# Performance work log

Hardware: AMD Instinct MI355X
Metric: run time of the kernel (lower is better)

## Reference

```python
import jax, jax.numpy as jnp
import numpy as np

N, D, E, L, H, F1, G, A = 4096, 256, 131072, 3, 4, 128, 16, 32

def setup_inputs() -> dict:
    key = jax.random.key(0)
    ks = jax.random.split(key, 12)
    s = lambda k, shape, fan: jax.random.normal(k, shape, jnp.float32) / np.sqrt(fan)
    return {
        "x": jax.random.normal(ks[0], (N, D), jnp.float32),
        "edge_attr": jax.random.uniform(ks[1], (E,), jnp.float32),
        "conv_Wself": s(ks[2], (L, D, D), D),
        "conv_Wnbr": s(ks[3], (L, D, D), D),
        "conv_b": jnp.zeros((L, D), jnp.float32),
        "bn_gamma": jnp.ones((L - 1, D), jnp.float32),
        "bn_beta": jnp.zeros((L - 1, D), jnp.float32),
        "bn_mean": jnp.zeros((L - 1, D), jnp.float32),
        "bn_var": jnp.ones((L - 1, D), jnp.float32),
        "Wqkv": s(ks[4], (3, D, D), D),
        "bqkv": jnp.zeros((3, D), jnp.float32),
        "Wo": s(ks[5], (D, D), D),
        "bo": jnp.zeros((D,), jnp.float32),
        "fc1_W": s(ks[6], (D, F1), D),
        "fc1_b": jnp.zeros((F1,), jnp.float32),
        "AW1": s(ks[7], (G, F1, A), F1),
        "Ab1": jnp.zeros((G, A), jnp.float32),
        "AW2": s(ks[8], (G, A, 1), A),
        "Ab2": jnp.zeros((G, 1), jnp.float32),
        "edge_index": jax.random.randint(ks[9], (2, E), 0, N, jnp.int32),
        "node_groups": jax.random.randint(ks[10], (N,), 0, G, jnp.int32),
    }


def reference(x, edge_attr, conv_Wself, conv_Wnbr, conv_b, bn_gamma, bn_beta,
              bn_mean, bn_var, Wqkv, bqkv, Wo, bo, fc1_W, fc1_b,
              AW1, Ab1, AW2, Ab2, edge_index, node_groups):
    src, dst = edge_index[0], edge_index[1]
    # message-passing conv stack (edge_attr only used by the last, non-attention layer)
    for i in range(L):
        msg = x[src]
        if i == L - 1:
            msg = msg * edge_attr[:, None]
        agg = jax.ops.segment_sum(msg, dst, num_segments=N)
        x = x @ conv_Wself[i] + agg @ conv_Wnbr[i] + conv_b[i]
        if i < L - 1:
            x = bn_gamma[i] * (x - bn_mean[i]) * jax.lax.rsqrt(bn_var[i] + 1e-5) + bn_beta[i]
            x = jax.nn.elu(x)
    # hierarchy self-attention over all N nodes (batch of 1), residual add
    dh = D // H
    q = (x @ Wqkv[0] + bqkv[0]).reshape(N, H, dh)
    k = (x @ Wqkv[1] + bqkv[1]).reshape(N, H, dh)
    v = (x @ Wqkv[2] + bqkv[2]).reshape(N, H, dh)
    scores = jnp.einsum('nhd,mhd->hnm', q, k) / np.sqrt(dh).astype(np.float32)
    attn = jax.nn.softmax(scores, axis=-1)
    o = jnp.einsum('hnm,mhd->nhd', attn, v).reshape(N, D) @ Wo + bo
    x = x + o
    feats = jax.nn.elu(x @ fc1_W + fc1_b)  # [N, F1]; dropout is eval no-op
    # MoE-style per-node group adapter routing: gather tiny MLP weights per node
    h = jax.nn.relu(jnp.einsum('nd,nda->na', feats, AW1[node_groups]) + Ab1[node_groups])
    out = jnp.einsum('na,nao->no', h, AW2[node_groups]) + Ab2[node_groups]  # [N, 1]
    return out
```

## Files before the change

kernel.cpp:

```cpp
#include <hip/hip_runtime.h>
#include <math.h>

#define NN   4096
#define DIM  256
#define NE   131072
#define NH   4
#define DH   64
#define F1D  128
#define NG   16
#define AD   32

typedef unsigned short u16;
typedef unsigned int   u32;
typedef _Float16 f16;
typedef __attribute__((ext_vector_type(8))) _Float16 half8;
typedef __attribute__((ext_vector_type(4))) float f32x4;

enum { EPI_BIAS = 0, EPI_BNELU = 1 };
enum { MEPI_WO = 0, MEPI_FC1 = 1 };

#define MFMA16(a, b, c) __builtin_amdgcn_mfma_f32_16x16x32_f16(a, b, c, 0, 0, 0)

__device__ inline u16 f2h(float x) { union { f16 f; u16 u; } c; c.f = (f16)x; return c.u; }
__device__ inline void split16(float x, u16& h, u16& l) {
    union { f16 f; u16 u; } ch, cl;
    ch.f = (f16)x;
    cl.f = (f16)(x - (float)ch.f);
    h = ch.u; l = cl.u;
}

__global__ void csr_count(const int* __restrict__ dst, int* __restrict__ cnt) {
    int e = blockIdx.x * 256 + threadIdx.x;
    atomicAdd(&cnt[dst[e]], 1);
}

__global__ __launch_bounds__(1024) void csr_scan(
    int* __restrict__ cnt, int* __restrict__ off)
{
    __shared__ int wsum[16];
    const int t = threadIdx.x;
    const int lane = t & 63;
    int4 v = *(const int4*)&cnt[t * 4];
    const int s = v.x + v.y + v.z + v.w;
    int acc = s;
    #pragma unroll
    for (int o = 1; o < 64; o <<= 1) {
        int u = __shfl_up(acc, o);
        if (lane >= o) acc += u;
    }
    if (lane == 63) wsum[t >> 6] = acc;
    __syncthreads();
    if (t < 16) {
        int w0 = wsum[t];
        int a2 = w0;
        #pragma unroll
        for (int o = 1; o < 16; o <<= 1) {
            int u = __shfl_up(a2, o);
            if (t >= o) a2 += u;
        }
        wsum[t] = a2 - w0;
    }
    __syncthreads();
    const int base = wsum[t >> 6] + (acc - s);
    off[t * 4 + 0] = base;
    off[t * 4 + 1] = base + v.x;
    off[t * 4 + 2] = base + v.x + v.y;
    off[t * 4 + 3] = base + v.x + v.y + v.z;
    *(int4*)&cnt[t * 4] = make_int4(0, 0, 0, 0);
    if (t == 1023) off[NN] = base + s;
}

__global__ void csr_fill(const int* __restrict__ dst, const int* __restrict__ src,
                         const float* __restrict__ eattr, const int* __restrict__ off,
                         int* __restrict__ cur, int* __restrict__ esrc,
                         float* __restrict__ ewt) {
    int e = blockIdx.x * 256 + threadIdx.x;
    int d = dst[e];
    int pos = off[d] + atomicAdd(&cur[d], 1);
    esrc[pos] = src[e];
    ewt[pos]  = eattr[e];
}

__global__ __launch_bounds__(256) void prep_kernel(
    const float* __restrict__ x,
    const float* __restrict__ Ws, const float* __restrict__ Wn,
    const float* __restrict__ Wqkv, const float* __restrict__ Wo,
    const float* __restrict__ fc1W,
    u16* __restrict__ xh, u16* __restrict__ xl,
    u16* __restrict__ wch, u16* __restrict__ wcl,
    u16* __restrict__ w4h, u16* __restrict__ w4l,
    u16* __restrict__ f1h, u16* __restrict__ f1l,
    int* __restrict__ cur)
{
    const int b = blockIdx.x;
    const int t = threadIdx.x;
    if (b < 1024) {
        const int gid = b * 256 + t;
        const float4 v = *(const float4*)&x[(size_t)gid * 4];
        u16 h[4], l[4];
        split16(v.x, h[0], l[0]); split16(v.y, h[1], l[1]);
        split16(v.z, h[2], l[2]); split16(v.w, h[3], l[3]);
        *(uint2*)&xh[(size_t)gid * 4] =
            make_uint2((u32)h[0] | ((u32)h[1] << 16), (u32)h[2] | ((u32)h[3] << 16));
        *(uint2*)&xl[(size_t)gid * 4] =
            make_uint2((u32)l[0] | ((u32)l[1] << 16), (u32)l[2] | ((u32)l[3] << 16));
    } else if (b < 1408) {
        const int gid = (b - 1024) * 256 + t;
        const int L = gid / 32768;
        const int rem = gid % 32768;
        const int m = rem / 128;
        const int k4 = (rem % 128) * 4;
        const float* S = Ws + (size_t)L * 65536;
        const float* Nb = Wn + (size_t)L * 65536;
        u16 h[4], l[4];
        #pragma unroll
        for (int j = 0; j < 4; ++j) {
            const int k = k4 + j;
            const float v = (k < 256) ? S[(size_t)k * 256 + m]
                                      : Nb[(size_t)(k - 256) * 256 + m];
            split16(v, h[j], l[j]);
        }
        const size_t o = (size_t)L * 131072 + (size_t)m * 512 + k4;
        *(uint2*)&wch[o] = make_uint2((u32)h[0] | ((u32)h[1] << 16), (u32)h[2] | ((u32)h[3] << 16));
        *(uint2*)&wcl[o] = make_uint2((u32)l[0] | ((u32)l[1] << 16), (u32)l[2] | ((u32)l[3] << 16));
    } else if (b < 1664) {
        const int gid = (b - 1408) * 256 + t;
        const int mat = gid / 16384;
        const int rem = gid % 16384;
        const int m = rem / 64;
        const int k4 = (rem % 64) * 4;
        const float* W = (mat < 3) ? Wqkv + (size_t)mat * 65536 : Wo;
        u16 h[4], l[4];
        #pragma unroll
        for (int j = 0; j < 4; ++j)
            split16(W[(size_t)(k4 + j) * 256 + m], h[j], l[j]);
        const size_t o = (size_t)mat * 65536 + (size_t)m * 256 + k4;
        *(uint2*)&w4h[o] = make_uint2((u32)h[0] | ((u32)h[1] << 16), (u32)h[2] | ((u32)h[3] << 16));
        *(uint2*)&w4l[o] = make_uint2((u32)l[0] | ((u32)l[1] << 16), (u32)l[2] | ((u32)l[3] << 16));
    } else if (b < 1696) {
        const int gid = (b - 1664) * 256 + t;
        const int m = gid / 64;
        const int k4 = (gid % 64) * 4;
        u16 h[4], l[4];
        #pragma unroll
        for (int j = 0; j < 4; ++j)
            split16(fc1W[(size_t)(k4 + j) * F1D + m], h[j], l[j]);
        const size_t o = (size_t)m * 256 + k4;
        *(uint2*)&f1h[o] = make_uint2((u32)h[0] | ((u32)h[1] << 16), (u32)h[2] | ((u32)h[3] << 16));
        *(uint2*)&f1l[o] = make_uint2((u32)l[0] | ((u32)l[1] << 16), (u32)l[2] | ((u32)l[3] << 16));
    } else {
        const int gid = (b - 1696) * 256 + t;
        if (gid < NN / 4) *(int4*)&cur[gid * 4] = make_int4(0, 0, 0, 0);
    }
}

template<bool LAST>
__global__ __launch_bounds__(256) void agg_kernel(
    const float* __restrict__ x, const int* __restrict__ esrc,
    const float* __restrict__ ewt, const int* __restrict__ off,
    u16* __restrict__ aggh, u16* __restrict__ aggl)
{
    const int node = blockIdx.x * 4 + (threadIdx.x >> 6);
    const int lane = threadIdx.x & 63;
    const int d4 = lane * 4;
    int j = off[node];
    const int j1 = off[node + 1];
    float4 acc = make_float4(0.f, 0.f, 0.f, 0.f);
    for (; j + 4 <= j1; j += 4) {
        const int s0 = esrc[j], s1 = esrc[j + 1], s2 = esrc[j + 2], s3 = esrc[j + 3];
        const float4 x0 = *(const float4*)&x[(size_t)s0 * DIM + d4];
        const float4 x1 = *(const float4*)&x[(size_t)s1 * DIM + d4];
        const float4 x2 = *(const float4*)&x[(size_t)s2 * DIM + d4];
        const float4 x3 = *(const float4*)&x[(size_t)s3 * DIM + d4];
        const float w0 = LAST ? ewt[j]     : 1.f;
        const float w1 = LAST ? ewt[j + 1] : 1.f;
        const float w2 = LAST ? ewt[j + 2] : 1.f;
        const float w3 = LAST ? ewt[j + 3] : 1.f;
        acc.x = fmaf(x0.x, w0, acc.x); acc.y = fmaf(x0.y, w0, acc.y);
        acc.z = fmaf(x0.z, w0, acc.z); acc.w = fmaf(x0.w, w0, acc.w);
        acc.x = fmaf(x1.x, w1, acc.x); acc.y = fmaf(x1.y, w1, acc.y);
        acc.z = fmaf(x1.z, w1, acc.z); acc.w = fmaf(x1.w, w1, acc.w);
        acc.x = fmaf(x2.x, w2, acc.x); acc.y = fmaf(x2.y, w2, acc.y);
        acc.z = fmaf(x2.z, w2, acc.z); acc.w = fmaf(x2.w, w2, acc.w);
        acc.x = fmaf(x3.x, w3, acc.x); acc.y = fmaf(x3.y, w3, acc.y);
        acc.z = fmaf(x3.z, w3, acc.z); acc.w = fmaf(x3.w, w3, acc.w);
    }
    for (; j < j1; ++j) {
        const int s = esrc[j];
        const float w = LAST ? ewt[j] : 1.f;
        const float4 xv = *(const float4*)&x[(size_t)s * DIM + d4];
        acc.x = fmaf(xv.x, w, acc.x); acc.y = fmaf(xv.y, w, acc.y);
        acc.z = fmaf(xv.z, w, acc.z); acc.w = fmaf(xv.w, w, acc.w);
    }
    u16 h[4], l[4];
    split16(acc.x, h[0], l[0]); split16(acc.y, h[1], l[1]);
    split16(acc.z, h[2], l[2]); split16(acc.w, h[3], l[3]);
    *(uint2*)&aggh[(size_t)node * DIM + d4] =
        make_uint2((u32)h[0] | ((u32)h[1] << 16), (u32)h[2] | ((u32)h[3] << 16));
    *(uint2*)&aggl[(size_t)node * DIM + d4] =
        make_uint2((u32)l[0] | ((u32)l[1] << 16), (u32)l[2] | ((u32)l[3] << 16));
}

template<int EPI>
__global__ __launch_bounds__(256) void conv_mfma(
    const u16* __restrict__ xh, const u16* __restrict__ xl,
    const u16* __restrict__ gh, const u16* __restrict__ gl,
    const u16* __restrict__ bth, const u16* __restrict__ btl,
    const float* __restrict__ bias,
    const float* __restrict__ gamma, const float* __restrict__ beta,
    const float* __restrict__ bnmean, const float* __restrict__ bnvar,
    float* __restrict__ outf, u16* __restrict__ oh, u16* __restrict__ ol)
{
    __shared__ u16 lds[13824];
    u16* As_h = lds;
    u16* As_l = lds + 2304;
    u16* Bs_h = lds + 4608;
    u16* Bs_l = lds + 9216;
    #define TKP 72

    const int tid  = threadIdx.x;
    const int row0 = blockIdx.y * 32;
    const int col0 = blockIdx.x * 64;

    const int w   = tid >> 6;
    const int l15 = tid & 15, h4 = (tid & 63) >> 4;
    const int rh  = w & 1, ch = w >> 1;
    const int arow = tid >> 3, acs = (tid & 7) * 8;
    const int brow = tid & 63, bseg = tid >> 6;
    const int bc = bseg * 16;

    uint4 sah, sal, sbh0, sbh1, sbl0, sbl1;
    {
        sah = *((const uint4*)&xh[(size_t)(row0 + arow) * DIM + acs]);
        sal = *((const uint4*)&xl[(size_t)(row0 + arow) * DIM + acs]);
        const u16* pbh = bth + (size_t)(col0 + brow) * 512 + bc;
        const u16* pbl = btl + (size_t)(col0 + brow) * 512 + bc;
        sbh0 = ((const uint4*)pbh)[0]; sbh1 = ((const uint4*)pbh)[1];
        sbl0 = ((const uint4*)pbl)[0]; sbl1 = ((const uint4*)pbl)[1];
    }

    const f32x4 z4 = {0.f, 0.f, 0.f, 0.f};
    f32x4 acc[2] = {z4, z4};

    for (int kt = 0; kt < 8; ++kt) {
        *(uint4*)&As_h[arow * TKP + acs] = sah;
        *(uint4*)&As_l[arow * TKP + acs] = sal;
        *(uint4*)&Bs_h[brow * TKP + bc]     = sbh0;
        *(uint4*)&Bs_h[brow * TKP + bc + 8] = sbh1;
        *(uint4*)&Bs_l[brow * TKP + bc]     = sbl0;
        *(uint4*)&Bs_l[brow * TKP + bc + 8] = sbl1;
        if (kt + 1 < 8) {
            const int kn = kt + 1;
            const u16 *pah, *pal;
            if (kn < 4) {
                pah = xh + (size_t)(row0 + arow) * DIM + kn * 64 + acs;
                pal = xl + (size_t)(row0 + arow) * DIM + kn * 64 + acs;
            } else {
                pah = gh + (size_t)(row0 + arow) * DIM + (kn - 4) * 64 + acs;
                pal = gl + (size_t)(row0 + arow) * DIM + (kn - 4) * 64 + acs;
            }
            sah = *((const uint4*)pah);
            sal = *((const uint4*)pal);
            const u16* pbh = bth + (size_t)(col0 + brow) * 512 + kn * 64 + bc;
            const u16* pbl = btl + (size_t)(col0 + brow) * 512 + kn * 64 + bc;
            sbh0 = ((const uint4*)pbh)[0]; sbh1 = ((const uint4*)pbh)[1];
            sbl0 = ((const uint4*)pbl)[0]; sbl1 = ((const uint4*)pbl)[1];
        }
        __syncthreads();

        __builtin_amdgcn_s_setprio(1);
        #pragma unroll
        for (int kc = 0; kc < 2; ++kc) {
            const int dc = kc * 32 + h4 * 8;
            half8 afh, afl, bfh[2], bfl[2];
            afh = *(const half8*)&As_h[(rh * 16 + l15) * TKP + dc];
            afl = *(const half8*)&As_l[(rh * 16 + l15) * TKP + dc];
            #pragma unroll
            for (int bb = 0; bb < 2; ++bb) {
                const int r = ch * 32 + bb * 16 + l15;
                bfh[bb] = *(const half8*)&Bs_h[r * TKP + dc];
                bfl[bb] = *(const half8*)&Bs_l[r * TKP + dc];
            }
            #pragma unroll
            for (int bb = 0; bb < 2; ++bb) {
                acc[bb] = MFMA16(afh, bfh[bb], acc[bb]);
                acc[bb] = MFMA16(afh, bfl[bb], acc[bb]);
                acc[bb] = MFMA16(afl, bfh[bb], acc[bb]);
            }
        }
        __builtin_amdgcn_s_setprio(0);
        __syncthreads();
    }

    #pragma unroll
    for (int bb = 0; bb < 2; ++bb) {
        const int c  = col0 + ch * 32 + bb * 16 + l15;
        const int r0 = row0 + rh * 16 + h4 * 4;
        #pragma unroll
        for (int i = 0; i < 4; ++i) {
            const int r = r0 + i;
            float t = acc[bb][i] + bias[c];
            if (EPI == EPI_BNELU) {
                t = gamma[c] * (t - bnmean[c]) * rsqrtf(bnvar[c] + 1e-5f) + beta[c];
                t = t > 0.f ? t : expm1f(t);
            }
            outf[(size_t)r * DIM + c] = t;
            u16 hh, ll;
            split16(t, hh, ll);
            oh[(size_t)r * DIM + c] = hh;
            ol[(size_t)r * DIM + c] = ll;
        }
    }
    #undef TKP
}

__global__ __launch_bounds__(256) void qkv_mfma(
    const u16* __restrict__ xh, const u16* __restrict__ xl,
    const u16* __restrict__ wth, const u16* __restrict__ wtl,
    const float* __restrict__ bias,
    u16* __restrict__ qh_o, u16* __restrict__ ql_o,
    u16* __restrict__ kh_o, u16* __restrict__ kl_o,
    u16* __restrict__ vt_o)
{
    __shared__ u16 lds[4 * 4608];
    u16* As_h = lds;
    u16* As_l = lds + 4608;
    u16* Bs_h = lds + 9216;
    u16* Bs_l = lds + 13824;
    #define TKP 72

    const int tid  = threadIdx.x;
    const int row0 = blockIdx.y * 64;
    const int mat  = blockIdx.x >> 2;
    const int col0 = (blockIdx.x & 3) * 64;
    const float* biasp = bias + mat * DIM;

    const int w   = tid >> 6;
    const int l15 = tid & 15, h4 = (tid & 63) >> 4;
    const int rh  = w & 1, ch = w >> 1;
    const int lrow = tid & 63, lseg = tid >> 6;
    const int lc = lseg * 16;

    const size_t brow = (size_t)(mat * 256 + col0 + lrow) * 256;
    uint4 sah0, sah1, sal0, sal1, sbh0, sbh1, sbl0, sbl1;
    {
        const u16* pah = xh + (size_t)(row0 + lrow) * DIM + lc;
        const u16* pal = xl + (size_t)(row0 + lrow) * DIM + lc;
        sah0 = ((const uint4*)pah)[0]; sah1 = ((const uint4*)pah)[1];
        sal0 = ((const uint4*)pal)[0]; sal1 = ((const uint4*)pal)[1];
        sbh0 = ((const uint4*)(wth + brow + lc))[0]; sbh1 = ((const uint4*)(wth + brow + lc))[1];
        sbl0 = ((const uint4*)(wtl + brow + lc))[0]; sbl1 = ((const uint4*)(wtl + brow + lc))[1];
    }

    const f32x4 z4 = {0.f, 0.f, 0.f, 0.f};
    f32x4 acc[2][2] = {{z4, z4}, {z4, z4}};

    for (int kt = 0; kt < 4; ++kt) {
        *(uint4*)&As_h[lrow * TKP + lc]     = sah0;
        *(uint4*)&As_h[lrow * TKP + lc + 8] = sah1;
        *(uint4*)&As_l[lrow * TKP + lc]     = sal0;
        *(uint4*)&As_l[lrow * TKP + lc + 8] = sal1;
        *(uint4*)&Bs_h[lrow * TKP + lc]     = sbh0;
        *(uint4*)&Bs_h[lrow * TKP + lc + 8] = sbh1;
        *(uint4*)&Bs_l[lrow * TKP + lc]     = sbl0;
        *(uint4*)&Bs_l[lrow * TKP + lc + 8] = sbl1;
        if (kt + 1 < 4) {
            const int kb = (kt + 1) * 64 + lc;
            const u16* pah = xh + (size_t)(row0 + lrow) * DIM + kb;
            const u16* pal = xl + (size_t)(row0 + lrow) * DIM + kb;
            sah0 = ((const uint4*)pah)[0]; sah1 = ((const uint4*)pah)[1];
            sal0 = ((const uint4*)pal)[0]; sal1 = ((const uint4*)pal)[1];
            sbh0 = ((const uint4*)(wth + brow + kb))[0]; sbh1 = ((const uint4*)(wth + brow + kb))[1];
            sbl0 = ((const uint4*)(wtl + brow + kb))[0]; sbl1 = ((const uint4*)(wtl + brow + kb))[1];
        }
        __syncthreads();

        __builtin_amdgcn_s_setprio(1);
        #pragma unroll
        for (int kc = 0; kc < 2; ++kc) {
            const int dc = kc * 32 + h4 * 8;
            half8 afh[2], afl[2], bfh[2], bfl[2];
            #pragma unroll
            for (int ab = 0; ab < 2; ++ab) {
                const int r = rh * 32 + ab * 16 + l15;
                afh[ab] = *(const half8*)&As_h[r * TKP + dc];
                afl[ab] = *(const half8*)&As_l[r * TKP + dc];
            }
            #pragma unroll
            for (int bb = 0; bb < 2; ++bb) {
                const int r = ch * 32 + bb * 16 + l15;
                bfh[bb] = *(const half8*)&Bs_h[r * TKP + dc];
                bfl[bb] = *(const half8*)&Bs_l[r * TKP + dc];
            }
            #pragma unroll
            for (int ab = 0; ab < 2; ++ab)
                #pragma unroll
                for (int bb = 0; bb < 2; ++bb) {
                    acc[ab][bb] = MFMA16(afh[ab], bfh[bb], acc[ab][bb]);
                    acc[ab][bb] = MFMA16(afh[ab], bfl[bb], acc[ab][bb]);
                    acc[ab][bb] = MFMA16(afl[ab], bfh[bb], acc[ab][bb]);
                }
        }
        __builtin_amdgcn_s_setprio(0);
        __syncthreads();
    }

    const float s = (mat == 0) ? 0.125f : 1.0f;
    u16* oph = (mat == 0) ? qh_o : kh_o;
    u16* opl = (mat == 0) ? ql_o : kl_o;
    #pragma unroll
    for (int ab = 0; ab < 2; ++ab)
        #pragma unroll
        for (int bb = 0; bb < 2; ++bb) {
            const int c  = col0 + ch * 32 + bb * 16 + l15;
            const int r0 = row0 + rh * 32 + ab * 16 + h4 * 4;
            if (mat < 2) {
                #pragma unroll
                for (int i = 0; i < 4; ++i) {
                    const int r = r0 + i;
                    const float t = (acc[ab][bb][i] + biasp[c]) * s;
                    u16 hh, ll;
                    split16(t, hh, ll);
                    oph[(size_t)r * DIM + c] = hh;
                    opl[(size_t)r * DIM + c] = ll;
                }
            } else {
                u16 v[4];
                #pragma unroll
                for (int i = 0; i < 4; ++i)
                    v[i] = f2h(acc[ab][bb][i] + biasp[c]);
                *(uint2*)&vt_o[(size_t)c * NN + r0] =
                    make_uint2((u32)v[0] | ((u32)v[1] << 16), (u32)v[2] | ((u32)v[3] << 16));
            }
        }
    #undef TKP
}

template<int MEPI>
__global__ __launch_bounds__(256) void mfma_gemm32(
    const u16* __restrict__ Ah, const u16* __restrict__ Al,
    const u16* __restrict__ Bth, const u16* __restrict__ Btl,
    const float* __restrict__ bias, const float* __restrict__ resid,
    float* __restrict__ outf, u16* __restrict__ outh, u16* __restrict__ outl,
    int K, int M)
{
    __shared__ u16 lds[13824];
    u16* As_h = lds;
    u16* As_l = lds + 2304;
    u16* Bs_h = lds + 4608;
    u16* Bs_l = lds + 9216;
    #define TKP 72

    const int tid  = threadIdx.x;
    const int row0 = blockIdx.y * 32;
    const int col0 = blockIdx.x * 64;

    const int w   = tid >> 6;
    const int l15 = tid & 15, h4 = (tid & 63) >> 4;
    const int rh  = w & 1, ch = w >> 1;
    const int arow = tid >> 3, acs = (tid & 7) * 8;
    const int brow = tid & 63, bseg = tid >> 6;
    const int bc = bseg * 16;

    uint4 sah, sal, sbh0, sbh1, sbl0, sbl1;
    {
        sah = *((const uint4*)&Ah[(size_t)(row0 + arow) * K + acs]);
        sal = *((const uint4*)&Al[(size_t)(row0 + arow) * K + acs]);
        const u16* pbh = Bth + (size_t)(col0 + brow) * K + bc;
        const u16* pbl = Btl + (size_t)(col0 + brow) * K + bc;
        sbh0 = ((const uint4*)pbh)[0]; sbh1 = ((const uint4*)pbh)[1];
        sbl0 = ((const uint4*)pbl)[0]; sbl1 = ((const uint4*)pbl)[1];
    }

    const f32x4 z4 = {0.f, 0.f, 0.f, 0.f};
    f32x4 acc[2] = {z4, z4};
    const int NKT2 = K / 64;

    for (int kt = 0; kt < NKT2; ++kt) {
        *(uint4*)&As_h[arow * TKP + acs] = sah;
        *(uint4*)&As_l[arow * TKP + acs] = sal;
        *(uint4*)&Bs_h[brow * TKP + bc]     = sbh0;
        *(uint4*)&Bs_h[brow * TKP + bc + 8] = sbh1;
        *(uint4*)&Bs_l[brow * TKP + bc]     = sbl0;
        *(uint4*)&Bs_l[brow * TKP + bc + 8] = sbl1;
        if (kt + 1 < NKT2) {
            const int kb = (kt + 1) * 64;
            sah = *((const uint4*)&Ah[(size_t)(row0 + arow) * K + kb + acs]);
            sal = *((const uint4*)&Al[(size_t)(row0 + arow) * K + kb + acs]);
            const u16* pbh = Bth + (size_t)(col0 + brow) * K + kb + bc;
            const u16* pbl = Btl + (size_t)(col0 + brow) * K + kb + bc;
            sbh0 = ((const uint4*)pbh)[0]; sbh1 = ((const uint4*)pbh)[1];
            sbl0 = ((const uint4*)pbl)[0]; sbl1 = ((const uint4*)pbl)[1];
        }
        __syncthreads();

        __builtin_amdgcn_s_setprio(1);
        #pragma unroll
        for (int kc = 0; kc < 2; ++kc) {
            const int dc = kc * 32 + h4 * 8;
            half8 afh, afl, bfh[2], bfl[2];
            afh = *(const half8*)&As_h[(rh * 16 + l15) * TKP + dc];
            afl = *(const half8*)&As_l[(rh * 16 + l15) * TKP + dc];
            #pragma unroll
            for (int bb = 0; bb < 2; ++bb) {
                const int r = ch * 32 + bb * 16 + l15;
                bfh[bb] = *(const half8*)&Bs_h[r * TKP + dc];
                bfl[bb] = *(const half8*)&Bs_l[r * TKP + dc];
            }
            #pragma unroll
            for (int bb = 0; bb < 2; ++bb) {
                acc[bb] = MFMA16(afh, bfh[bb], acc[bb]);
                acc[bb] = MFMA16(afh, bfl[bb], acc[bb]);
                acc[bb] = MFMA16(afl, bfh[bb], acc[bb]);
            }
        }
        __builtin_amdgcn_s_setprio(0);
        __syncthreads();
    }

    #pragma unroll
    for (int bb = 0; bb < 2; ++bb) {
        const int c  = col0 + ch * 32 + bb * 16 + l15;
        const int r0 = row0 + rh * 16 + h4 * 4;
        #pragma unroll
        for (int i = 0; i < 4; ++i) {
            const int r = r0 + i;
            float t = acc[bb][i] + bias[c];
            if (MEPI == MEPI_WO) {
                t += resid[(size_t)r * M + c];
                u16 hh, ll;
                split16(t, hh, ll);
                outh[(size_t)r * M + c] = hh;
                outl[(size_t)r * M + c] = ll;
            } else {
                t = t > 0.f ? t : expm1f(t);
                outf[(size_t)r * M + c] = t;
            }
        }
    }
    #undef TKP
}

#define QB 128
#define KB 64
#define NSPLIT 4
#define NKT (NN / KB)
#define KP 72

__global__ __launch_bounds__(512, 2) void attn_kernel(
    const u16* __restrict__ qhi, const u16* __restrict__ qlo,
    const u16* __restrict__ khi, const u16* __restrict__ klo,
    const u16* __restrict__ vT,
    float* __restrict__ op0, float* __restrict__ op1,
    float* __restrict__ op2, float* __restrict__ op3,
    float* __restrict__ mpart, float* __restrict__ lpart)
{
    __shared__ u16 lds[27648];
    u16* Kh0 = lds;
    u16* Kl0 = lds + 4608;
    u16* Vt0 = lds + 9216;
    u16* Kh1 = lds + 13824;
    u16* Kl1 = lds + 18432;
    u16* Vt1 = lds + 23040;
    u16* Qh  = lds;
    u16* Ql  = lds + 13824;

    const int tid = threadIdx.x;
    const int h   = blockIdx.y;
    const int q0  = blockIdx.x * QB;
    const int sp  = blockIdx.z;
    const int kt0 = sp * (NKT / NSPLIT);
    const int kt1 = kt0 + NKT / NSPLIT;

    const int w   = tid >> 6;
    const int l15 = tid & 15, h4 = (tid & 63) >> 4;
    const int lrow = tid & 63, lseg = tid >> 6;
    const int gq8 = h * DH + lseg * 8;

    {
        const int qrow = tid >> 2, qseg = tid & 3;
        const u16* s0 = qhi + (size_t)(q0 + qrow) * DIM + h * DH + qseg * 16;
        const u16* s1 = qlo + (size_t)(q0 + qrow) * DIM + h * DH + qseg * 16;
        uint4 a = ((const uint4*)s0)[0], b = ((const uint4*)s0)[1];
        uint4 c = ((const uint4*)s1)[0], d = ((const uint4*)s1)[1];
        *(uint4*)&Qh[qrow * KP + qseg * 16]     = a;
        *(uint4*)&Qh[qrow * KP + qseg * 16 + 8] = b;
        *(uint4*)&Ql[qrow * KP + qseg * 16]     = c;
        *(uint4*)&Ql[qrow * KP + qseg * 16 + 8] = d;
    }

    uint4 rk, rl, rv;
    auto load_tile = [&](int kt_ld) {
        const int key0 = kt_ld * KB;
        rk = *(const uint4*)(khi + (size_t)(key0 + lrow) * DIM + gq8);
        rl = *(const uint4*)(klo + (size_t)(key0 + lrow) * DIM + gq8);
        rv = *(const uint4*)(vT + (size_t)(h * DH + lrow) * NN + key0 + lseg * 8);
    };
    load_tile(kt0);
    __syncthreads();

    half8 qf[2][2];
    #pragma unroll
    for (int kc = 0; kc < 2; ++kc) {
        const int r = w * 16 + l15;
        const int dc = kc * 32 + h4 * 8;
        qf[kc][0] = *(const half8*)&Qh[r * KP + dc];
        qf[kc][1] = *(const half8*)&Ql[r * KP + dc];
    }
    __syncthreads();

    auto stage_to = [&](u16* Kh, u16* Kl, u16* Vt) {
        *(uint4*)&Kh[lrow * KP + lseg * 8] = rk;
        *(uint4*)&Kl[lrow * KP + lseg * 8] = rl;
        *(uint4*)&Vt[lrow * KP + lseg * 8] = rv;
    };

    stage_to(Kh0, Kl0, Vt0);
    load_tile(kt0 + 1);
    __syncthreads();

    const f32x4 z4 = {0.f, 0.f, 0.f, 0.f};
    f32x4 oacc[4] = {z4, z4, z4, z4};
    float m_run = -3.0e38f, l_run = 0.f;
    const int sl0 = (h4 & 1) * 32 + l15;
    const int sl1 = sl0 + 16;

    auto tile_body = [&](int t, u16* Kc, u16* Lc, u16* Vc,
                         u16* Kn, u16* Ln, u16* Vn) {
        if (t + 1 < kt1) stage_to(Kn, Ln, Vn);
        if (t + 2 < kt1) load_tile(t + 2);

        f32x4 sc[4] = {z4, z4, z4, z4};
        __builtin_amdgcn_s_setprio(1);
        #pragma unroll
        for (int kc = 0; kc < 2; ++kc) {
            const int dc = kc * 32 + h4 * 8;
            half8 kfh[4], kfl[4];
            #pragma unroll
            for (int kcb = 0; kcb < 4; ++kcb) {
                const int r = kcb * 16 + l15;
                kfh[kcb] = *(const half8*)&Kc[r * KP + dc];
                kfl[kcb] = *(const half8*)&Lc[r * KP + dc];
            }
            #pragma unroll
            for (int kcb = 0; kcb < 4; ++kcb) {
                sc[kcb] = MFMA16(kfh[kcb], qf[kc][0], sc[kcb]);
                sc[kcb] = MFMA16(kfl[kcb], qf[kc][0], sc[kcb]);
                sc[kcb] = MFMA16(kfh[kcb], qf[kc][1], sc[kcb]);
            }
        }
        __builtin_amdgcn_s_setprio(0);

        float c0 = fmaxf(fmaxf(sc[0][0], sc[0][1]), fmaxf(sc[0][2], sc[0][3]));
        float c1 = fmaxf(fmaxf(sc[1][0], sc[1][1]), fmaxf(sc[1][2], sc[1][3]));
        float c2 = fmaxf(fmaxf(sc[2][0], sc[2][1]), fmaxf(sc[2][2], sc[2][3]));
        float c3 = fmaxf(fmaxf(sc[3][0], sc[3][1]), fmaxf(sc[3][2], sc[3][3]));
        float pm = fmaxf(fmaxf(c0, c1), fmaxf(c2, c3));
        pm = fmaxf(pm, __shfl_xor(pm, 16));
        pm = fmaxf(pm, __shfl_xor(pm, 32));

        float p[4][4];
        float base, fr = 1.f;
        int resc;
        if (__all(pm - m_run <= 8.f)) {
            base = m_run;
            resc = 0;
        } else {
            const float mnew = fmaxf(m_run, pm);
            fr = __expf(m_run - mnew);
            m_run = mnew;
            base = mnew;
            resc = 1;
        }
        #pragma unroll
        for (int kcb = 0; kcb < 4; ++kcb)
            #pragma unroll
            for (int i = 0; i < 4; ++i)
                p[kcb][i] = __expf(sc[kcb][i] - base);
        float s0s = (p[0][0] + p[0][1]) + (p[0][2] + p[0][3]);
        float s1s = (p[1][0] + p[1][1]) + (p[1][2] + p[1][3]);
        float s2s = (p[2][0] + p[2][1]) + (p[2][2] + p[2][3]);
        float s3s = (p[3][0] + p[3][1]) + (p[3][2] + p[3][3]);
        float ls = (s0s + s1s) + (s2s + s3s);
        ls += __shfl_xor(ls, 16);
        ls += __shfl_xor(ls, 32);
        if (resc) {
            l_run = l_run * fr + ls;
            #pragma unroll
            for (int db = 0; db < 4; ++db) oacc[db] *= fr;
        } else {
            l_run += ls;
        }

        u32 pk01[4], pk23[4];
        #pragma unroll
        for (int kcb = 0; kcb < 4; ++kcb) {
            pk01[kcb] = (u32)f2h(p[kcb][0]) | ((u32)f2h(p[kcb][1]) << 16);
            pk23[kcb] = (u32)f2h(p[kcb][2]) | ((u32)f2h(p[kcb][3]) << 16);
        }

        const int hiSel = h4 >> 1;
        __builtin_amdgcn_s_setprio(1);
        #pragma unroll
        for (int kc = 0; kc < 2; ++kc) {
            const u32 a0 = (u32)__shfl((int)pk01[kc * 2], sl0);
            const u32 a1 = (u32)__shfl((int)pk23[kc * 2], sl0);
            const u32 a2 = (u32)__shfl((int)pk01[kc * 2], sl1);
            const u32 a3 = (u32)__shfl((int)pk23[kc * 2], sl1);
            const u32 b0 = (u32)__shfl((int)pk01[kc * 2 + 1], sl0);
            const u32 b1 = (u32)__shfl((int)pk23[kc * 2 + 1], sl0);
            const u32 b2 = (u32)__shfl((int)pk01[kc * 2 + 1], sl1);
            const u32 b3 = (u32)__shfl((int)pk23[kc * 2 + 1], sl1);
            union { half8 v; u32 u[4]; } pf;
            pf.u[0] = hiSel ? b0 : a0;
            pf.u[1] = hiSel ? b1 : a1;
            pf.u[2] = hiSel ? b2 : a2;
            pf.u[3] = hiSel ? b3 : a3;
            #pragma unroll
            for (int db = 0; db < 4; ++db) {
                const half8 vf = *(const half8*)&Vc[(db * 16 + l15) * KP + kc * 32 + h4 * 8];
                oacc[db] = MFMA16(vf, pf.v, oacc[db]);
            }
        }
        __builtin_amdgcn_s_setprio(0);
        __syncthreads();
    };

    for (int t = kt0; t < kt1; t += 2) {
        tile_body(t,     Kh0, Kl0, Vt0, Kh1, Kl1, Vt1);
        tile_body(t + 1, Kh1, Kl1, Vt1, Kh0, Kl0, Vt0);
    }

    float* ob = (sp == 0) ? op0 : ((sp == 1) ? op1 : ((sp == 2) ? op2 : op3));
    #pragma unroll
    for (int db = 0; db < 4; ++db)
        *(f32x4*)&ob[(size_t)(q0 + w * 16 + l15) * DIM + h * DH + db * 16 + h4 * 4] = oacc[db];
    if (h4 == 0) {
        const int r = w * 16 + l15;
        mpart[((size_t)sp * NN + q0 + r) * NH + h] = m_run;
        lpart[((size_t)sp * NN + q0 + r) * NH + h] = l_run;
    }
}

__global__ __launch_bounds__(256) void attn_combine(
    const float* __restrict__ o0, const float* __restrict__ o1,
    const float* __restrict__ o2, const float* __restrict__ o3,
    const float* __restrict__ mp, const float* __restrict__ lp,
    u16* __restrict__ ohi, u16* __restrict__ olo)
{
    const int gid = blockIdx.x * 256 + threadIdx.x;
    const int row = gid >> 6;
    const int c4  = (gid & 63) * 4;
    const int h   = c4 >> 6;
    float m[4], wgt[4];
    #pragma unroll
    for (int z = 0; z < 4; ++z) m[z] = mp[((size_t)z * NN + row) * NH + h];
    const float M = fmaxf(fmaxf(m[0], m[1]), fmaxf(m[2], m[3]));
    float den = 0.f;
    #pragma unroll
    for (int z = 0; z < 4; ++z) {
        wgt[z] = __expf(m[z] - M);
        den += lp[((size_t)z * NN + row) * NH + h] * wgt[z];
    }
    const float inv = 1.f / den;
    const float4 a = *(const float4*)&o0[(size_t)row * DIM + c4];
    const float4 b = *(const float4*)&o1[(size_t)row * DIM + c4];
    const float4 c = *(const float4*)&o2[(size_t)row * DIM + c4];
    const float4 d = *(const float4*)&o3[(size_t)row * DIM + c4];
    float r[4];
    r[0] = (a.x * wgt[0] + b.x * wgt[1] + c.x * wgt[2] + d.x * wgt[3]) * inv;
    r[1] = (a.y * wgt[0] + b.y * wgt[1] + c.y * wgt[2] + d.y * wgt[3]) * inv;
    r[2] = (a.z * wgt[0] + b.z * wgt[1] + c.z * wgt[2] + d.z * wgt[3]) * inv;
    r[3] = (a.w * wgt[0] + b.w * wgt[1] + c.w * wgt[2] + d.w * wgt[3]) * inv;
    u16 hh[4], ll[4];
    #pragma unroll
    for (int j = 0; j < 4; ++j) split16(r[j], hh[j], ll[j]);
    *(uint2*)&ohi[(size_t)row * DIM + c4] =
        make_uint2((u32)hh[0] | ((u32)hh[1] << 16), (u32)hh[2] | ((u32)hh[3] << 16));
    *(uint2*)&olo[(size_t)row * DIM + c4] =
        make_uint2((u32)ll[0] | ((u32)ll[1] << 16), (u32)ll[2] | ((u32)ll[3] << 16));
}

__global__ __launch_bounds__(256) void adapter_kernel(
    const float* __restrict__ feats, const int* __restrict__ grp,
    const float* __restrict__ AW1, const float* __restrict__ Ab1,
    const float* __restrict__ AW2, const float* __restrict__ Ab2,
    float* __restrict__ out)
{
    const int wv = threadIdx.x >> 6;
    const int n = blockIdx.x * 4 + wv;
    const int lane = threadIdx.x & 63;
    __shared__ float f[4][F1D];
    f[wv][lane]      = feats[(size_t)n * F1D + lane];
    f[wv][lane + 64] = feats[(size_t)n * F1D + 64 + lane];
    const int g = grp[n];
    const float* W1 = AW1 + (size_t)g * F1D * AD;
    const int a = lane & 31;
    const int half = lane >> 5;
    float hsum = 0.f;
    for (int d = 0; d < 64; ++d)
        hsum = fmaf(f[wv][half * 64 + d], W1[(half * 64 + d) * AD + a], hsum);
    hsum += __shfl_xor(hsum, 32);
    hsum = fmaxf(hsum + Ab1[g * AD + a], 0.f);
    float p = hsum * AW2[g * AD + a];
    #pragma unroll
    for (int mm = 1; mm < 32; mm <<= 1) p += __shfl_xor(p, mm);
    if (lane == 0) out[n] = p + Ab2[g];
}

extern "C" void kernel_launch(void* const* d_in, const int* in_sizes, int n_in,
                              void* d_out, int out_size, void* d_ws, size_t ws_size,
                              hipStream_t stream)
{
    const float* x_in   = (const float*)d_in[0];
    const float* eattr  = (const float*)d_in[1];
    const float* Wself  = (const float*)d_in[2];
    const float* Wnbr   = (const float*)d_in[3];
    const float* convb  = (const float*)d_in[4];
    const float* gamma  = (const float*)d_in[5];
    const float* beta   = (const float*)d_in[6];
    const float* bnmean = (const float*)d_in[7];
    const float* bnvar  = (const float*)d_in[8];
    const float* Wqkv   = (const float*)d_in[9];
    const float* bqkv   = (const float*)d_in[10];
    const float* Wo     = (const float*)d_in[11];
    const float* bo     = (const float*)d_in[12];
    const float* fc1W   = (const float*)d_in[13];
    const float* fc1b   = (const float*)d_in[14];
    const float* AW1    = (const float*)d_in[15];
    const float* Ab1    = (const float*)d_in[16];
    const float* AW2    = (const float*)d_in[17];
    const float* Ab2    = (const float*)d_in[18];
    const int*   eidx   = (const int*)d_in[19];
    const int*   grp    = (const int*)d_in[20];
    const int* srcArr = eidx;
    const int* dstArr = eidx + NE;

    float* fws = (float*)d_ws;
    const size_t NM = (size_t)NN * DIM;
    float* bufA  = fws;
    float* bufB  = fws + NM;
    float* bufC  = fws + 2 * NM;
    float* feats = fws + 3 * NM;
    float* mpart = fws + 3 * NM + NM / 2;
    float* lpart = mpart + 4 * NN * NH;
    u16* up = (u16*)(lpart + 4 * NN * NH);
    u16* xpAh = up;             u16* xpAl = xpAh + NM;
    u16* xpBh = xpAl + NM;      u16* xpBl = xpBh + NM;
    u16* aggh = xpBl + NM;      u16* aggl = aggh + NM;
    u16* qh = aggl + NM;        u16* ql = qh + NM;
    u16* kh = ql + NM;          u16* kl = kh + NM;
    u16* vt = kl + NM;
    u16* wcath = vt + NM;
    u16* wcatl = wcath + 3 * 131072;
    u16* wt4h  = wcatl + 3 * 131072;
    u16* wt4l  = wt4h + 4 * 65536;
    u16* fc1h  = wt4l + 4 * 65536;
    u16* fc1l  = fc1h + 32768;
    int*   esrc = (int*)(fc1l + 32768);
    float* ewt  = (float*)(esrc + NE);
    int* off    = (int*)(ewt + NE);
    int* cur    = off + NN + 1;
    float* outp = (float*)d_out;

    float* op2 = (float*)xpAh;
    float* op3 = (float*)xpBh;

    prep_kernel<<<1700, 256, 0, stream>>>(
        x_in, Wself, Wnbr, Wqkv, Wo, fc1W,
        xpAh, xpAl, wcath, wcatl, wt4h, wt4l, fc1h, fc1l, cur);

    csr_count<<<NE / 256, 256, 0, stream>>>(dstArr, cur);
    csr_scan<<<1, 1024, 0, stream>>>(cur, off);
    csr_fill<<<NE / 256, 256, 0, stream>>>(dstArr, srcArr, eattr, off, cur, esrc, ewt);

    const dim3 gc(DIM / 64, NN / 32);
    const int rgrid = NN * DIM / 4 / 256;

    agg_kernel<false><<<NN / 4, 256, 0, stream>>>(x_in, esrc, ewt, off, aggh, aggl);
    conv_mfma<EPI_BNELU><<<gc, 256, 0, stream>>>(
        xpAh, xpAl, aggh, aggl, wcath, wcatl, convb,
        gamma, beta, bnmean, bnvar, bufA, xpBh, xpBl);
    agg_kernel<false><<<NN / 4, 256, 0, stream>>>(bufA, esrc, ewt, off, aggh, aggl);
    conv_mfma<EPI_BNELU><<<gc, 256, 0, stream>>>(
        xpBh, xpBl, aggh, aggl, wcath + 131072, wcatl + 131072, convb + DIM,
        gamma + DIM, beta + DIM, bnmean + DIM, bnvar + DIM, bufC, xpAh, xpAl);
    agg_kernel<true><<<NN / 4, 256, 0, stream>>>(bufC, esrc, ewt, off, aggh, aggl);
    conv_mfma<EPI_BIAS><<<gc, 256, 0, stream>>>(
        xpAh, xpAl, aggh, aggl, wcath + 262144, wcatl + 262144, convb + 2 * DIM,
        nullptr, nullptr, nullptr, nullptr, bufA, xpBh, xpBl);

    qkv_mfma<<<dim3(12, NN / 64), 256, 0, stream>>>(
        xpBh, xpBl, wt4h, wt4l, bqkv, qh, ql, kh, kl, vt);

    attn_kernel<<<dim3(NN / QB, NH, NSPLIT), 512, 0, stream>>>(
        qh, ql, kh, kl, vt, bufB, bufC, op2, op3, mpart, lpart);
    attn_combine<<<rgrid, 256, 0, stream>>>(
        bufB, bufC, op2, op3, mpart, lpart, qh, ql);

    mfma_gemm32<MEPI_WO><<<dim3(DIM / 64, NN / 32), 256, 0, stream>>>(
        qh, ql, wt4h + 3 * 65536, wt4l + 3 * 65536, bo, bufA,
        nullptr, kh, kl, DIM, DIM);

    mfma_gemm32<MEPI_FC1><<<dim3(F1D / 64, NN / 32), 256, 0, stream>>>(
        kh, kl, fc1h, fc1l, fc1b, nullptr, feats, nullptr, nullptr, DIM, F1D);

    adapter_kernel<<<NN / 4, 256, 0, stream>>>(feats, grp, AW1, Ab1, AW2, Ab2, outp);
}
```

Baseline: 211.6 us.

## Split attention keys six ways, XOR-swizzle LDS tiles, store normalized fp16 partials

The attention split-K factor goes from 4 to 6 so the grid has more blocks, and the loop now handles an uneven tile count per split by swapping buffers after each tile instead of unrolling by two. The padded LDS layout (row stride 72) is replaced with an unpadded 64-wide layout using an XOR swizzle, which shrinks LDS use and is meant to avoid bank conflicts. Each split now stores its partial output already normalized and packed as fp16 rather than fp32, which halves partial write and read traffic. The combine kernel reweights the six partials using l times exp(m minus M). The fp16 partials lose some precision, and six splits mean more combine work and more redundant Q loads.

```diff
diff --git a/kernel.cpp b/kernel.cpp
--- a/kernel.cpp
+++ b/kernel.cpp
@@ -22,11 +22,15 @@
 #define MFMA16(a, b, c) __builtin_amdgcn_mfma_f32_16x16x32_f16(a, b, c, 0, 0, 0)
 
 __device__ inline u16 f2h(float x) { union { f16 f; u16 u; } c; c.f = (f16)x; return c.u; }
+__device__ inline float h2f(u16 h) { union { f16 f; u16 u; } c; c.u = h; return (float)c.f; }
 __device__ inline void split16(float x, u16& h, u16& l) {
     union { f16 f; u16 u; } ch, cl;
     ch.f = (f16)x;
     cl.f = (f16)(x - (float)ch.f);
     h = ch.u; l = cl.u;
+}
+__device__ inline int swz64(int row, int colByte) {
+    return row * 64 + ((colByte ^ ((row & 7) << 4)) >> 1);
 }
 
 __global__ void csr_count(const int* __restrict__ dst, int* __restrict__ cnt) {
@@ -543,34 +547,33 @@
 
 #define QB 128
 #define KB 64
-#define NSPLIT 4
+#define NSPLIT 6
 #define NKT (NN / KB)
-#define KP 72
 
 __global__ __launch_bounds__(512, 2) void attn_kernel(
     const u16* __restrict__ qhi, const u16* __restrict__ qlo,
     const u16* __restrict__ khi, const u16* __restrict__ klo,
     const u16* __restrict__ vT,
-    float* __restrict__ op0, float* __restrict__ op1,
-    float* __restrict__ op2, float* __restrict__ op3,
+    u16* __restrict__ op0, u16* __restrict__ op1, u16* __restrict__ op2,
+    u16* __restrict__ op3, u16* __restrict__ op4, u16* __restrict__ op5,
     float* __restrict__ mpart, float* __restrict__ lpart)
 {
-    __shared__ u16 lds[27648];
+    __shared__ u16 lds[24576];
     u16* Kh0 = lds;
-    u16* Kl0 = lds + 4608;
-    u16* Vt0 = lds + 9216;
-    u16* Kh1 = lds + 13824;
-    u16* Kl1 = lds + 18432;
-    u16* Vt1 = lds + 23040;
+    u16* Kl0 = lds + 4096;
+    u16* Vt0 = lds + 8192;
+    u16* Kh1 = lds + 12288;
+    u16* Kl1 = lds + 16384;
+    u16* Vt1 = lds + 20480;
     u16* Qh  = lds;
-    u16* Ql  = lds + 13824;
+    u16* Ql  = lds + 8192;
 
     const int tid = threadIdx.x;
     const int h   = blockIdx.y;
     const int q0  = blockIdx.x * QB;
     const int sp  = blockIdx.z;
-    const int kt0 = sp * (NKT / NSPLIT);
-    const int kt1 = kt0 + NKT / NSPLIT;
+    const int kt0 = (sp * NKT) / NSPLIT;
+    const int kt1 = ((sp + 1) * NKT) / NSPLIT;
 
     const int w   = tid >> 6;
     const int l15 = tid & 15, h4 = (tid & 63) >> 4;
@@ -583,10 +586,10 @@
         const u16* s1 = qlo + (size_t)(q0 + qrow) * DIM + h * DH + qseg * 16;
         uint4 a = ((const uint4*)s0)[0], b = ((const uint4*)s0)[1];
         uint4 c = ((const uint4*)s1)[0], d = ((const uint4*)s1)[1];
-        *(uint4*)&Qh[qrow * KP + qseg * 16]     = a;
-        *(uint4*)&Qh[qrow * KP + qseg * 16 + 8] = b;
-        *(uint4*)&Ql[qrow * KP + qseg * 16]     = c;
-        *(uint4*)&Ql[qrow * KP + qseg * 16 + 8] = d;
+        *(uint4*)&Qh[swz64(qrow, qseg * 32)]      = a;
+        *(uint4*)&Qh[swz64(qrow, qseg * 32 + 16)] = b;
+        *(uint4*)&Ql[swz64(qrow, qseg * 32)]      = c;
+        *(uint4*)&Ql[swz64(qrow, qseg * 32 + 16)] = d;
     }
 
     uint4 rk, rl, rv;
@@ -603,16 +606,17 @@
     #pragma unroll
     for (int kc = 0; kc < 2; ++kc) {
         const int r = w * 16 + l15;
-        const int dc = kc * 32 + h4 * 8;
-        qf[kc][0] = *(const half8*)&Qh[r * KP + dc];
-        qf[kc][1] = *(const half8*)&Ql[r * KP + dc];
+        const int cb = kc * 64 + h4 * 16;
+        qf[kc][0] = *(const half8*)&Qh[swz64(r, cb)];
+        qf[kc][1] = *(const half8*)&Ql[swz64(r, cb)];
     }
     __syncthreads();
 
     auto stage_to = [&](u16* Kh, u16* Kl, u16* Vt) {
-        *(uint4*)&Kh[lrow * KP + lseg * 8] = rk;
-        *(uint4*)&Kl[lrow * KP + lseg * 8] = rl;
-        *(uint4*)&Vt[lrow * KP + lseg * 8] = rv;
+        const int idx = swz64(lrow, lseg * 16);
+        *(uint4*)&Kh[idx] = rk;
+        *(uint4*)&Kl[idx] = rl;
+        *(uint4*)&Vt[idx] = rv;
     };
 
     stage_to(Kh0, Kl0, Vt0);
@@ -634,13 +638,14 @@
         __builtin_amdgcn_s_setprio(1);
         #pragma unroll
         for (int kc = 0; kc < 2; ++kc) {
-            const int dc = kc * 32 + h4 * 8;
+            const int cb = kc * 64 + h4 * 16;
             half8 kfh[4], kfl[4];
             #pragma unroll
             for (int kcb = 0; kcb < 4; ++kcb) {
                 const int r = kcb * 16 + l15;
-                kfh[kcb] = *(const half8*)&Kc[r * KP + dc];
-                kfl[kcb] = *(const half8*)&Lc[r * KP + dc];
+                const int idx = swz64(r, cb);
+                kfh[kcb] = *(const half8*)&Kc[idx];
+                kfl[kcb] = *(const half8*)&Lc[idx];
             }
             #pragma unroll
             for (int kcb = 0; kcb < 4; ++kcb) {
@@ -716,9 +721,10 @@
             pf.u[1] = hiSel ? b1 : a1;
             pf.u[2] = hiSel ? b2 : a2;
             pf.u[3] = hiSel ? b3 : a3;
+            const int cb = kc * 64 + h4 * 16;
             #pragma unroll
             for (int db = 0; db < 4; ++db) {
-                const half8 vf = *(const half8*)&Vc[(db * 16 + l15) * KP + kc * 32 + h4 * 8];
+                const half8 vf = *(const half8*)&Vc[swz64(db * 16 + l15, cb)];
                 oacc[db] = MFMA16(vf, pf.v, oacc[db]);
             }
         }
@@ -726,15 +732,28 @@
         __syncthreads();
     };
 
-    for (int t = kt0; t < kt1; t += 2) {
-        tile_body(t,     Kh0, Kl0, Vt0, Kh1, Kl1, Vt1);
-        tile_body(t + 1, Kh1, Kl1, Vt1, Kh0, Kl0, Vt0);
-    }
-
-    float* ob = (sp == 0) ? op0 : ((sp == 1) ? op1 : ((sp == 2) ? op2 : op3));
-    #pragma unroll
-    for (int db = 0; db < 4; ++db)
-        *(f32x4*)&ob[(size_t)(q0 + w * 16 + l15) * DIM + h * DH + db * 16 + h4 * 4] = oacc[db];
+    {
+        u16 *Kc = Kh0, *Lc = Kl0, *Vc = Vt0;
+        u16 *Kn = Kh1, *Ln = Kl1, *Vn = Vt1;
+        for (int t = kt0; t < kt1; ++t) {
+            tile_body(t, Kc, Lc, Vc, Kn, Ln, Vn);
+            u16* tmp;
+            tmp = Kc; Kc = Kn; Kn = tmp;
+            tmp = Lc; Lc = Ln; Ln = tmp;
+            tmp = Vc; Vc = Vn; Vn = tmp;
+        }
+    }
+
+    u16* ob = (sp == 0) ? op0 : ((sp == 1) ? op1 : ((sp == 2) ? op2 :
+              ((sp == 3) ? op3 : ((sp == 4) ? op4 : op5))));
+    const float inv = 1.f / l_run;
+    #pragma unroll
+    for (int db = 0; db < 4; ++db) {
+        u32 w0 = (u32)f2h(oacc[db][0] * inv) | ((u32)f2h(oacc[db][1] * inv) << 16);
+        u32 w1 = (u32)f2h(oacc[db][2] * inv) | ((u32)f2h(oacc[db][3] * inv) << 16);
+        *(uint2*)&ob[(size_t)(q0 + w * 16 + l15) * DIM + h * DH + db * 16 + h4 * 4] =
+            make_uint2(w0, w1);
+    }
     if (h4 == 0) {
         const int r = w * 16 + l15;
         mpart[((size_t)sp * NN + q0 + r) * NH + h] = m_run;
@@ -743,8 +762,9 @@
 }
 
 __global__ __launch_bounds__(256) void attn_combine(
-    const float* __restrict__ o0, const float* __restrict__ o1,
-    const float* __restrict__ o2, const float* __restrict__ o3,
+    const u16* __restrict__ o0, const u16* __restrict__ o1,
+    const u16* __restrict__ o2, const u16* __restrict__ o3,
+    const u16* __restrict__ o4, const u16* __restrict__ o5,
     const float* __restrict__ mp, const float* __restrict__ lp,
     u16* __restrict__ ohi, u16* __restrict__ olo)
 {
@@ -752,29 +772,32 @@
     const int row = gid >> 6;
     const int c4  = (gid & 63) * 4;
     const int h   = c4 >> 6;
-    float m[4], wgt[4];
-    #pragma unroll
-    for (int z = 0; z < 4; ++z) m[z] = mp[((size_t)z * NN + row) * NH + h];
-    const float M = fmaxf(fmaxf(m[0], m[1]), fmaxf(m[2], m[3]));
+    float m[6], wgt[6];
+    #pragma unroll
+    for (int z = 0; z < 6; ++z) m[z] = mp[((size_t)z * NN + row) * NH + h];
+    float M = m[0];
+    #pragma unroll
+    for (int z = 1; z < 6; ++z) M = fmaxf(M, m[z]);
     float den = 0.f;
     #pragma unroll
-    for (int z = 0; z < 4; ++z) {
-        wgt[z] = __expf(m[z] - M);
-        den += lp[((size_t)z * NN + row) * NH + h] * wgt[z];
+    for (int z = 0; z < 6; ++z) {
+        wgt[z] = lp[((size_t)z * NN + row) * NH + h] * __expf(m[z] - M);
+        den += wgt[z];
     }
     const float inv = 1.f / den;
-    const float4 a = *(const float4*)&o0[(size_t)row * DIM + c4];
-    const float4 b = *(const float4*)&o1[(size_t)row * DIM + c4];
-    const float4 c = *(const float4*)&o2[(size_t)row * DIM + c4];
-    const float4 d = *(const float4*)&o3[(size_t)row * DIM + c4];
-    float r[4];
-    r[0] = (a.x * wgt[0] + b.x * wgt[1] + c.x * wgt[2] + d.x * wgt[3]) * inv;
-    r[1] = (a.y * wgt[0] + b.y * wgt[1] + c.y * wgt[2] + d.y * wgt[3]) * inv;
-    r[2] = (a.z * wgt[0] + b.z * wgt[1] + c.z * wgt[2] + d.z * wgt[3]) * inv;
-    r[3] = (a.w * wgt[0] + b.w * wgt[1] + c.w * wgt[2] + d.w * wgt[3]) * inv;
+    const u16* ps[6] = {o0, o1, o2, o3, o4, o5};
+    float r[4] = {0.f, 0.f, 0.f, 0.f};
+    #pragma unroll
+    for (int z = 0; z < 6; ++z) {
+        const uint2 v = *(const uint2*)&ps[z][(size_t)row * DIM + c4];
+        r[0] += wgt[z] * h2f((u16)(v.x & 0xffff));
+        r[1] += wgt[z] * h2f((u16)(v.x >> 16));
+        r[2] += wgt[z] * h2f((u16)(v.y & 0xffff));
+        r[3] += wgt[z] * h2f((u16)(v.y >> 16));
+    }
     u16 hh[4], ll[4];
     #pragma unroll
-    for (int j = 0; j < 4; ++j) split16(r[j], hh[j], ll[j]);
+    for (int j = 0; j < 4; ++j) split16(r[j] * inv, hh[j], ll[j]);
     *(uint2*)&ohi[(size_t)row * DIM + c4] =
         make_uint2((u32)hh[0] | ((u32)hh[1] << 16), (u32)hh[2] | ((u32)hh[3] << 16));
     *(uint2*)&olo[(size_t)row * DIM + c4] =
@@ -843,8 +866,8 @@
     float* bufC  = fws + 2 * NM;
     float* feats = fws + 3 * NM;
     float* mpart = fws + 3 * NM + NM / 2;
-    float* lpart = mpart + 4 * NN * NH;
-    u16* up = (u16*)(lpart + 4 * NN * NH);
+    float* lpart = mpart + 6 * NN * NH;
+    u16* up = (u16*)(lpart + 6 * NN * NH);
     u16* xpAh = up;             u16* xpAl = xpAh + NM;
     u16* xpBh = xpAl + NM;      u16* xpBl = xpBh + NM;
     u16* aggh = xpBl + NM;      u16* aggl = aggh + NM;
@@ -863,8 +886,12 @@
     int* cur    = off + NN + 1;
     float* outp = (float*)d_out;
 
-    float* op2 = (float*)xpAh;
-    float* op3 = (float*)xpBh;
+    u16* o0 = (u16*)bufB;
+    u16* o1 = (u16*)bufC;
+    u16* o2 = xpAh;
+    u16* o3 = xpBh;
+    u16* o4 = aggh;
+    u16* o5 = (u16*)feats;
 
     prep_kernel<<<1700, 256, 0, stream>>>(
         x_in, Wself, Wnbr, Wqkv, Wo, fc1W,
@@ -894,9 +921,9 @@
         xpBh, xpBl, wt4h, wt4l, bqkv, qh, ql, kh, kl, vt);
 
     attn_kernel<<<dim3(NN / QB, NH, NSPLIT), 512, 0, stream>>>(
-        qh, ql, kh, kl, vt, bufB, bufC, op2, op3, mpart, lpart);
+        qh, ql, kh, kl, vt, o0, o1, o2, o3, o4, o5, mpart, lpart);
     attn_combine<<<rgrid, 256, 0, stream>>>(
-        bufB, bufC, op2, op3, mpart, lpart, qh, ql);
+        o0, o1, o2, o3, o4, o5, mpart, lpart, qh, ql);
 
     mfma_gemm32<MEPI_WO><<<dim3(DIM / 64, NN / 32), 256, 0, stream>>>(
         qh, ql, wt4h + 3 * 65536, wt4l + 3 * 65536, bo, bufA,
```

Measured after the change: 211.5 us. No clear change (-0.1%).
